# Kernel optimization log

Hardware: AMD Instinct MI355X
Metric: run time of the kernel (lower is better)

The kernel has to match this reference:

```python
import jax, jax.numpy as jnp
import numpy as np

H_Q = 32      # num_attention_heads
H_KV = 8      # num_key_value_heads
D = 128       # head_dim
WIN = 127     # left window size (flash window_size=(127,-1))
BLK = 128


def setup_inputs() -> dict:
    key = jax.random.key(0)
    kq, kk, kv = jax.random.split(key, 3)
    B, S = 2, 4096
    Q = jax.random.normal(kq, (B, S, H_Q * D), dtype=jnp.float32)
    K = jax.random.normal(kk, (B, S, H_KV * D), dtype=jnp.float32)
    V = jax.random.normal(kv, (B, S, H_KV * D), dtype=jnp.float32)
    return {"Q": Q, "K": K, "V": V}


def _banded_mask(nblk):
    # query row r in block n has global index n*BLK + r
    # key col c in window indexes global key (n-1)*BLK + c,  c in [0, 2*BLK)
    r = jnp.arange(BLK)[:, None]
    c = jnp.arange(2 * BLK)[None, :]
    base = (c <= r + BLK) & (c >= r + BLK - WIN)          # [BLK, 2BLK]
    n = jnp.arange(nblk)[:, None, None]
    valid_pad = (n > 0) | (c[None] >= BLK)                # block 0 has zero-padded left keys
    return base[None] & valid_pad                          # [nblk, BLK, 2BLK]


def reference(Q, K, V):
    B, S, _ = Q.shape
    nblk = S // BLK
    g = H_Q // H_KV
    scale = 1.0 / np.sqrt(D)

    # [B, Hkv, g, nblk, BLK, D]
    q = Q.reshape(B, S, H_Q, D).transpose(0, 2, 1, 3).reshape(B, H_KV, g, nblk, BLK, D)
    k = K.reshape(B, S, H_KV, D).transpose(0, 2, 1, 3)   # [B, Hkv, S, D]
    v = V.reshape(B, S, H_KV, D).transpose(0, 2, 1, 3)

    # pad one zero block in front, then build 2-block sliding windows
    pad = jnp.zeros((B, H_KV, BLK, D), dtype=K.dtype)
    kp = jnp.concatenate([pad, k], axis=2).reshape(B, H_KV, nblk + 1, BLK, D)
    vp = jnp.concatenate([pad, v], axis=2).reshape(B, H_KV, nblk + 1, BLK, D)
    kwin = jnp.concatenate([kp[:, :, :-1], kp[:, :, 1:]], axis=3)  # [B,Hkv,nblk,2BLK,D]
    vwin = jnp.concatenate([vp[:, :, :-1], vp[:, :, 1:]], axis=3)

    scores = jnp.einsum('bhgnrd,bhncd->bhgnrc', q, kwin) * scale   # [B,Hkv,g,nblk,BLK,2BLK]
    mask = _banded_mask(nblk)                                      # [nblk,BLK,2BLK]
    scores = jnp.where(mask[None, None, None], scores, jnp.finfo(scores.dtype).min)
    p = jax.nn.softmax(scores, axis=-1)
    out = jnp.einsum('bhgnrc,bhncd->bhgnrd', p, vwin)              # [B,Hkv,g,nblk,BLK,D]
    out = out.reshape(B, H_Q, S, D).transpose(0, 2, 1, 3).reshape(B, S, H_Q * D)
    return out
```

## Files before the change

kernel.cpp:

```cpp
#include <hip/hip_runtime.h>
#include <stdint.h>

#define S_LEN 4096
#define HQ 32
#define HKV 8
#define DD 128
#define QBLK 128
#define KVROW (HKV * DD)

typedef __attribute__((ext_vector_type(8)))  __bf16 bf16x8;
typedef __attribute__((ext_vector_type(2)))  __bf16 bf16x2;
typedef __attribute__((ext_vector_type(4)))  float  f32x4;
typedef __attribute__((ext_vector_type(2)))  unsigned int u32x2;
typedef __attribute__((ext_vector_type(4)))  unsigned int u32x4;

__device__ __forceinline__ unsigned int pk2(float lo, float hi2) {
  bf16x2 t = {(__bf16)lo, (__bf16)hi2};
  return __builtin_bit_cast(unsigned int, t);
}
__device__ __forceinline__ bf16x8 mk8(unsigned int w0, unsigned int w1,
                                      unsigned int w2, unsigned int w3) {
  u32x4 u = {w0, w1, w2, w3};
  return __builtin_bit_cast(bf16x8, u);
}

#define SWZV(d) ((((d) & 7) ^ (((d) >> 4) & 7)) << 3)

__global__ __launch_bounds__(512, 4)
void swa_fwd(const float* __restrict__ Qg, const float* __restrict__ Kg,
             const float* __restrict__ Vg, float* __restrict__ Og) {
  __shared__ __align__(16) unsigned char Kl[40960];
  __shared__ __align__(16) unsigned char Vl[40960];

  const int nwg  = gridDim.x;
  const int bid0 = blockIdx.x;
  const int bid  = (bid0 & 7) * (nwg >> 3) + (bid0 >> 3);

  const int j    = bid & 3;
  const int n    = (bid >> 2) & 31;
  const int hkv  = (bid >> 7) & 7;
  const int b    = bid >> 10;
  const int tid  = threadIdx.x;
  const int lane = tid & 63;
  const int wv   = tid >> 6;
  const int g    = lane >> 4;
  const int l15  = lane & 15;

  const int cc = wv & 1;
  const int h  = hkv * 4 + (wv >> 1);
  const int cg = 2 * j + cc;
  const int qrow = n * QBLK + 32 * j + cc * 16 + l15;

  const float* qp = Qg + (size_t)(b * S_LEN + qrow) * (HQ * DD) + h * DD + g * 8;
  bf16x8 qf[4];
  #pragma unroll
  for (int dc = 0; dc < 4; ++dc) {
    f32x4 a  = *(const f32x4*)(qp + dc * 32);
    f32x4 c4 = *(const f32x4*)(qp + dc * 32 + 4);
    qf[dc] = mk8(pk2(a[0], a[1]), pk2(a[2], a[3]),
                 pk2(c4[0], c4[1]), pk2(c4[2], c4[3]));
  }

  const int kbase = (n - 1) * QBLK + 32 * j;
  const int c0 = tid >> 5;
  const int dc = tid & 31;
  f32x4 xk[10], xv[10];
  #pragma unroll
  for (int i = 0; i < 10; ++i) {
    int tk = kbase + c0 + i * 16;
    tk = tk > 0 ? tk : 0;
    const size_t base = (size_t)(b * S_LEN + tk) * KVROW + hkv * DD + dc * 4;
    xk[i] = *(const f32x4*)(Kg + base);
    xv[i] = *(const f32x4*)(Vg + base);
  }
  #pragma unroll
  for (int i = 0; i < 10; ++i) {
    const int c = c0 + i * 16;
    u32x2 kw = { pk2(xk[i][0], xk[i][1]), pk2(xk[i][2], xk[i][3]) };
    *(u32x2*)(&Kl[c * 256 + ((dc * 8) ^ (c0 << 4))]) = kw;
    #pragma unroll
    for (int j4 = 0; j4 < 4; ++j4) {
      const int d = dc * 4 + j4;
      *(unsigned short*)(&Vl[d * 320 + ((c * 2) ^ SWZV(d))]) =
          __builtin_bit_cast(unsigned short, (__bf16)xv[i][j4]);
    }
  }
  __syncthreads();

  const float SC = 0.08838834764831845f * 1.44269504088896340f;

  f32x4 o[8];
  #pragma unroll
  for (int dt = 0; dt < 8; ++dt) o[dt] = (f32x4){0.f, 0.f, 0.f, 0.f};
  float ls = 0.f;

  #pragma unroll
  for (int pp = 0; pp < 5; ++pp) {
    const int tt0 = 2 * pp, tt1 = 2 * pp + 1;
    if (n == 0 && cg + tt1 < 8) continue;

    unsigned int w0 = 0, w1 = 0, w2 = 0, w3 = 0;

    if (!(n == 0 && cg + tt0 < 8)) {
      const int c = (cc + tt0) * 16 + l15;
      f32x4 acc = {0.f, 0.f, 0.f, 0.f};
      __builtin_amdgcn_s_setprio(1);
      #pragma unroll
      for (int dcc = 0; dcc < 4; ++dcc) {
        const bf16x8 kf = *(const bf16x8*)(
            &Kl[c * 256 + ((dcc * 64 + g * 16) ^ ((c & 15) << 4))]);
        acc = __builtin_amdgcn_mfma_f32_16x16x32_bf16(kf, qf[dcc], acc, 0, 0, 0);
      }
      __builtin_amdgcn_s_setprio(0);
      float p[4];
      #pragma unroll
      for (int r = 0; r < 4; ++r) {
        const int g4r = g * 4 + r;
        const float e = __builtin_amdgcn_exp2f(acc[r] * SC);
        bool valid = true;
        if (pp == 0) valid = (g4r > l15);
        if (pp == 4) valid = (g4r <= l15);
        p[r] = valid ? e : 0.f;
        ls += p[r];
      }
      w0 = pk2(p[0], p[1]);
      w1 = pk2(p[2], p[3]);
    }

    if (pp < 4 && !(n == 0 && cg + tt1 < 8)) {
      const int c = (cc + tt1) * 16 + l15;
      f32x4 acc = {0.f, 0.f, 0.f, 0.f};
      __builtin_amdgcn_s_setprio(1);
      #pragma unroll
      for (int dcc = 0; dcc < 4; ++dcc) {
        const bf16x8 kf = *(const bf16x8*)(
            &Kl[c * 256 + ((dcc * 64 + g * 16) ^ ((c & 15) << 4))]);
        acc = __builtin_amdgcn_mfma_f32_16x16x32_bf16(kf, qf[dcc], acc, 0, 0, 0);
      }
      __builtin_amdgcn_s_setprio(0);
      float p0 = __builtin_amdgcn_exp2f(acc[0] * SC);
      float p1 = __builtin_amdgcn_exp2f(acc[1] * SC);
      float p2 = __builtin_amdgcn_exp2f(acc[2] * SC);
      float p3 = __builtin_amdgcn_exp2f(acc[3] * SC);
      ls += p0 + p1 + p2 + p3;
      w2 = pk2(p0, p1);
      w3 = pk2(p2, p3);
    }

    const bf16x8 pf = mk8(w0, w1, w2, w3);
    const int ck0 = ((cc + tt0) * 16 + g * 4) * 2;
    const int ck1 = (pp < 4) ? ((cc + tt1) * 16 + g * 4) * 2 : ck0;
    __builtin_amdgcn_s_setprio(1);
    #pragma unroll
    for (int dt = 0; dt < 8; ++dt) {
      const int d  = dt * 16 + l15;
      const int rb = d * 320;
      const int sz = SWZV(d);
      const u32x2 a0 = *(const u32x2*)(&Vl[rb + (ck0 ^ sz)]);
      const u32x2 a1 = *(const u32x2*)(&Vl[rb + (ck1 ^ sz)]);
      const bf16x8 vf = mk8(a0[0], a0[1], a1[0], a1[1]);
      o[dt] = __builtin_amdgcn_mfma_f32_16x16x32_bf16(vf, pf, o[dt], 0, 0, 0);
    }
    __builtin_amdgcn_s_setprio(0);
  }

  ls += __shfl_xor(ls, 16);
  ls += __shfl_xor(ls, 32);
  const float inv = 1.0f / ls;

  float* op = Og + (size_t)(b * S_LEN + qrow) * (HQ * DD) + h * DD + g * 4;
  #pragma unroll
  for (int dt = 0; dt < 8; ++dt) {
    f32x4 v = o[dt];
    v[0] *= inv; v[1] *= inv; v[2] *= inv; v[3] *= inv;
    *(f32x4*)(op + dt * 16) = v;
  }
}

extern "C" void kernel_launch(void* const* d_in, const int* in_sizes, int n_in,
                              void* d_out, int out_size, void* d_ws, size_t ws_size,
                              hipStream_t stream) {
  const float* Q = (const float*)d_in[0];
  const float* K = (const float*)d_in[1];
  const float* V = (const float*)d_in[2];
  float* O = (float*)d_out;
  const int B = in_sizes[0] / (S_LEN * HQ * DD);
  const int nblocks = B * HKV * (S_LEN / QBLK) * 4;
  swa_fwd<<<dim3(nblocks), dim3(512), 0, stream>>>(Q, K, V, O);
}
```

Measured before the change: 87.23 us.

## Split K/V staging in two halves and overlap second load with compute

The K/V tile load is split into two halves. The first half is converted and stored to LDS before any compute starts. The second half's global loads are issued right after the first barrier and stay in flight while the first two score/PV pair iterations run on already-staged rows; they are then written to LDS behind a second barrier before the remaining pairs. This aims to hide global-memory latency behind MFMA work, at the cost of an extra block barrier and roughly 40 extra live VGPRs during compute under a tight launch bound.

```diff
diff --git a/kernel.cpp b/kernel.cpp
--- a/kernel.cpp
+++ b/kernel.cpp
@@ -54,38 +54,50 @@
   const float* qp = Qg + (size_t)(b * S_LEN + qrow) * (HQ * DD) + h * DD + g * 8;
   bf16x8 qf[4];
   #pragma unroll
-  for (int dc = 0; dc < 4; ++dc) {
-    f32x4 a  = *(const f32x4*)(qp + dc * 32);
-    f32x4 c4 = *(const f32x4*)(qp + dc * 32 + 4);
-    qf[dc] = mk8(pk2(a[0], a[1]), pk2(a[2], a[3]),
-                 pk2(c4[0], c4[1]), pk2(c4[2], c4[3]));
+  for (int dc4 = 0; dc4 < 4; ++dc4) {
+    f32x4 a  = *(const f32x4*)(qp + dc4 * 32);
+    f32x4 c4 = *(const f32x4*)(qp + dc4 * 32 + 4);
+    qf[dc4] = mk8(pk2(a[0], a[1]), pk2(a[2], a[3]),
+                  pk2(c4[0], c4[1]), pk2(c4[2], c4[3]));
   }
 
   const int kbase = (n - 1) * QBLK + 32 * j;
   const int c0 = tid >> 5;
   const int dc = tid & 31;
-  f32x4 xk[10], xv[10];
-  #pragma unroll
-  for (int i = 0; i < 10; ++i) {
+  const size_t kvoff = hkv * DD + dc * 4;
+
+  f32x4 xk0[5], xv0[5];
+  #pragma unroll
+  for (int i = 0; i < 5; ++i) {
     int tk = kbase + c0 + i * 16;
     tk = tk > 0 ? tk : 0;
-    const size_t base = (size_t)(b * S_LEN + tk) * KVROW + hkv * DD + dc * 4;
-    xk[i] = *(const f32x4*)(Kg + base);
-    xv[i] = *(const f32x4*)(Vg + base);
-  }
-  #pragma unroll
-  for (int i = 0; i < 10; ++i) {
+    const size_t base = (size_t)(b * S_LEN + tk) * KVROW + kvoff;
+    xk0[i] = *(const f32x4*)(Kg + base);
+    xv0[i] = *(const f32x4*)(Vg + base);
+  }
+  #pragma unroll
+  for (int i = 0; i < 5; ++i) {
     const int c = c0 + i * 16;
-    u32x2 kw = { pk2(xk[i][0], xk[i][1]), pk2(xk[i][2], xk[i][3]) };
+    u32x2 kw = { pk2(xk0[i][0], xk0[i][1]), pk2(xk0[i][2], xk0[i][3]) };
     *(u32x2*)(&Kl[c * 256 + ((dc * 8) ^ (c0 << 4))]) = kw;
     #pragma unroll
     for (int j4 = 0; j4 < 4; ++j4) {
       const int d = dc * 4 + j4;
       *(unsigned short*)(&Vl[d * 320 + ((c * 2) ^ SWZV(d))]) =
-          __builtin_bit_cast(unsigned short, (__bf16)xv[i][j4]);
+          __builtin_bit_cast(unsigned short, (__bf16)xv0[i][j4]);
     }
   }
   __syncthreads();
+
+  f32x4 xk1[5], xv1[5];
+  #pragma unroll
+  for (int i = 0; i < 5; ++i) {
+    int tk = kbase + c0 + (i + 5) * 16;
+    tk = tk > 0 ? tk : 0;
+    const size_t base = (size_t)(b * S_LEN + tk) * KVROW + kvoff;
+    xk1[i] = *(const f32x4*)(Kg + base);
+    xv1[i] = *(const f32x4*)(Vg + base);
+  }
 
   const float SC = 0.08838834764831845f * 1.44269504088896340f;
 
@@ -94,75 +106,98 @@
   for (int dt = 0; dt < 8; ++dt) o[dt] = (f32x4){0.f, 0.f, 0.f, 0.f};
   float ls = 0.f;
 
-  #pragma unroll
-  for (int pp = 0; pp < 5; ++pp) {
-    const int tt0 = 2 * pp, tt1 = 2 * pp + 1;
-    if (n == 0 && cg + tt1 < 8) continue;
-
-    unsigned int w0 = 0, w1 = 0, w2 = 0, w3 = 0;
-
-    if (!(n == 0 && cg + tt0 < 8)) {
-      const int c = (cc + tt0) * 16 + l15;
-      f32x4 acc = {0.f, 0.f, 0.f, 0.f};
-      __builtin_amdgcn_s_setprio(1);
-      #pragma unroll
-      for (int dcc = 0; dcc < 4; ++dcc) {
-        const bf16x8 kf = *(const bf16x8*)(
-            &Kl[c * 256 + ((dcc * 64 + g * 16) ^ ((c & 15) << 4))]);
-        acc = __builtin_amdgcn_mfma_f32_16x16x32_bf16(kf, qf[dcc], acc, 0, 0, 0);
-      }
-      __builtin_amdgcn_s_setprio(0);
-      float p[4];
-      #pragma unroll
-      for (int r = 0; r < 4; ++r) {
-        const int g4r = g * 4 + r;
-        const float e = __builtin_amdgcn_exp2f(acc[r] * SC);
-        bool valid = true;
-        if (pp == 0) valid = (g4r > l15);
-        if (pp == 4) valid = (g4r <= l15);
-        p[r] = valid ? e : 0.f;
-        ls += p[r];
-      }
-      w0 = pk2(p[0], p[1]);
-      w1 = pk2(p[2], p[3]);
+#define PAIR_BODY(pp)                                                         \
+  {                                                                           \
+    const int tt0 = 2 * (pp), tt1 = 2 * (pp) + 1;                             \
+    if (!(n == 0 && cg + tt1 < 8)) {                                          \
+      unsigned int w0 = 0, w1 = 0, w2 = 0, w3 = 0;                            \
+      if (!(n == 0 && cg + tt0 < 8)) {                                        \
+        const int c = (cc + tt0) * 16 + l15;                                  \
+        f32x4 acc = {0.f, 0.f, 0.f, 0.f};                                     \
+        __builtin_amdgcn_s_setprio(1);                                        \
+        _Pragma("unroll")                                                     \
+        for (int dcc = 0; dcc < 4; ++dcc) {                                   \
+          const bf16x8 kf = *(const bf16x8*)(                                 \
+              &Kl[c * 256 + ((dcc * 64 + g * 16) ^ ((c & 15) << 4))]);        \
+          acc = __builtin_amdgcn_mfma_f32_16x16x32_bf16(kf, qf[dcc], acc,     \
+                                                        0, 0, 0);             \
+        }                                                                     \
+        __builtin_amdgcn_s_setprio(0);                                        \
+        float p[4];                                                           \
+        _Pragma("unroll")                                                     \
+        for (int r = 0; r < 4; ++r) {                                         \
+          const int g4r = g * 4 + r;                                          \
+          const float e = __builtin_amdgcn_exp2f(acc[r] * SC);                \
+          bool valid = true;                                                  \
+          if ((pp) == 0) valid = (g4r > l15);                                 \
+          if ((pp) == 4) valid = (g4r <= l15);                                \
+          p[r] = valid ? e : 0.f;                                             \
+          ls += p[r];                                                         \
+        }                                                                     \
+        w0 = pk2(p[0], p[1]);                                                 \
+        w1 = pk2(p[2], p[3]);                                                 \
+      }                                                                       \
+      if ((pp) < 4 && !(n == 0 && cg + tt1 < 8)) {                            \
+        const int c = (cc + tt1) * 16 + l15;                                  \
+        f32x4 acc = {0.f, 0.f, 0.f, 0.f};                                     \
+        __builtin_amdgcn_s_setprio(1);                                        \
+        _Pragma("unroll")                                                     \
+        for (int dcc = 0; dcc < 4; ++dcc) {                                   \
+          const bf16x8 kf = *(const bf16x8*)(                                 \
+              &Kl[c * 256 + ((dcc * 64 + g * 16) ^ ((c & 15) << 4))]);        \
+          acc = __builtin_amdgcn_mfma_f32_16x16x32_bf16(kf, qf[dcc], acc,     \
+                                                        0, 0, 0);             \
+        }                                                                     \
+        __builtin_amdgcn_s_setprio(0);                                        \
+        float p0 = __builtin_amdgcn_exp2f(acc[0] * SC);                       \
+        float p1 = __builtin_amdgcn_exp2f(acc[1] * SC);                       \
+        float p2 = __builtin_amdgcn_exp2f(acc[2] * SC);                       \
+        float p3 = __builtin_amdgcn_exp2f(acc[3] * SC);                       \
+        ls += p0 + p1 + p2 + p3;                                              \
+        w2 = pk2(p0, p1);                                                     \
+        w3 = pk2(p2, p3);                                                     \
+      }                                                                       \
+      const bf16x8 pf = mk8(w0, w1, w2, w3);                                  \
+      const int ck0 = ((cc + tt0) * 16 + g * 4) * 2;                          \
+      const int ck1 = ((pp) < 4) ? ((cc + tt1) * 16 + g * 4) * 2 : ck0;       \
+      __builtin_amdgcn_s_setprio(1);                                          \
+      _Pragma("unroll")                                                       \
+      for (int dt = 0; dt < 8; ++dt) {                                        \
+        const int d  = dt * 16 + l15;                                         \
+        const int rb = d * 320;                                               \
+        const int sz = SWZV(d);                                               \
+        const u32x2 a0 = *(const u32x2*)(&Vl[rb + (ck0 ^ sz)]);               \
+        const u32x2 a1 = *(const u32x2*)(&Vl[rb + (ck1 ^ sz)]);               \
+        const bf16x8 vf = mk8(a0[0], a0[1], a1[0], a1[1]);                    \
+        o[dt] = __builtin_amdgcn_mfma_f32_16x16x32_bf16(vf, pf, o[dt],        \
+                                                        0, 0, 0);             \
+      }                                                                       \
+      __builtin_amdgcn_s_setprio(0);                                          \
+    }                                                                         \
+  }
+
+  PAIR_BODY(0)
+  PAIR_BODY(1)
+
+  __builtin_amdgcn_sched_barrier(0);
+  #pragma unroll
+  for (int i = 0; i < 5; ++i) {
+    const int c = c0 + (i + 5) * 16;
+    u32x2 kw = { pk2(xk1[i][0], xk1[i][1]), pk2(xk1[i][2], xk1[i][3]) };
+    *(u32x2*)(&Kl[c * 256 + ((dc * 8) ^ (c0 << 4))]) = kw;
+    #pragma unroll
+    for (int j4 = 0; j4 < 4; ++j4) {
+      const int d = dc * 4 + j4;
+      *(unsigned short*)(&Vl[d * 320 + ((c * 2) ^ SWZV(d))]) =
+          __builtin_bit_cast(unsigned short, (__bf16)xv1[i][j4]);
     }
-
-    if (pp < 4 && !(n == 0 && cg + tt1 < 8)) {
-      const int c = (cc + tt1) * 16 + l15;
-      f32x4 acc = {0.f, 0.f, 0.f, 0.f};
-      __builtin_amdgcn_s_setprio(1);
-      #pragma unroll
-      for (int dcc = 0; dcc < 4; ++dcc) {
-        const bf16x8 kf = *(const bf16x8*)(
-            &Kl[c * 256 + ((dcc * 64 + g * 16) ^ ((c & 15) << 4))]);
-        acc = __builtin_amdgcn_mfma_f32_16x16x32_bf16(kf, qf[dcc], acc, 0, 0, 0);
-      }
-      __builtin_amdgcn_s_setprio(0);
-      float p0 = __builtin_amdgcn_exp2f(acc[0] * SC);
-      float p1 = __builtin_amdgcn_exp2f(acc[1] * SC);
-      float p2 = __builtin_amdgcn_exp2f(acc[2] * SC);
-      float p3 = __builtin_amdgcn_exp2f(acc[3] * SC);
-      ls += p0 + p1 + p2 + p3;
-      w2 = pk2(p0, p1);
-      w3 = pk2(p2, p3);
-    }
-
-    const bf16x8 pf = mk8(w0, w1, w2, w3);
-    const int ck0 = ((cc + tt0) * 16 + g * 4) * 2;
-    const int ck1 = (pp < 4) ? ((cc + tt1) * 16 + g * 4) * 2 : ck0;
-    __builtin_amdgcn_s_setprio(1);
-    #pragma unroll
-    for (int dt = 0; dt < 8; ++dt) {
-      const int d  = dt * 16 + l15;
-      const int rb = d * 320;
-      const int sz = SWZV(d);
-      const u32x2 a0 = *(const u32x2*)(&Vl[rb + (ck0 ^ sz)]);
-      const u32x2 a1 = *(const u32x2*)(&Vl[rb + (ck1 ^ sz)]);
-      const bf16x8 vf = mk8(a0[0], a0[1], a1[0], a1[1]);
-      o[dt] = __builtin_amdgcn_mfma_f32_16x16x32_bf16(vf, pf, o[dt], 0, 0, 0);
-    }
-    __builtin_amdgcn_s_setprio(0);
-  }
+  }
+  __syncthreads();
+
+  PAIR_BODY(2)
+  PAIR_BODY(3)
+  PAIR_BODY(4)
+#undef PAIR_BODY
 
   ls += __shfl_xor(ls, 16);
   ls += __shfl_xor(ls, 32);
```

Result: faster. 85.00 us (-2.6%).
